# Optimization experiments

Measured on AMD Instinct MI355X. Metric: run time of the kernel, lower is better.

The kernel has to match this reference:

```python
import jax, jax.numpy as jnp
import numpy as np

SCORE_THRESHOLD = 0.5
IOU_THRESHOLD = 0.5
N = 8192
IMG = 640.0


def setup_inputs() -> dict:
    key = jax.random.key(0)
    k1, k2, k3 = jax.random.split(key, 3)
    # valid xyxy boxes on a 640px canvas: x2 > x1, y2 > y1
    xy1 = jax.random.uniform(k1, (N, 2), dtype=jnp.float32) * (IMG - 64.0)
    wh = jax.random.uniform(k2, (N, 2), dtype=jnp.float32) * 96.0 + 4.0
    xyxy = jnp.concatenate([xy1, xy1 + wh], axis=1)  # [N,4]
    person_conf = jax.random.uniform(k3, (N,), dtype=jnp.float32)  # [N]
    return {"xyxy": xyxy, "person_conf": person_conf}


def _pairwise_iou(boxes):
    # boxes: [N,4] xyxy -> iou: [N,N]
    x1, y1, x2, y2 = boxes[:, 0], boxes[:, 1], boxes[:, 2], boxes[:, 3]
    area = (x2 - x1) * (y2 - y1)  # [N]
    ix1 = jnp.maximum(x1[:, None], x1[None, :])
    iy1 = jnp.maximum(y1[:, None], y1[None, :])
    ix2 = jnp.minimum(x2[:, None], x2[None, :])
    iy2 = jnp.minimum(y2[:, None], y2[None, :])
    iw = jnp.maximum(ix2 - ix1, 0.0)
    ih = jnp.maximum(iy2 - iy1, 0.0)
    inter = iw * ih
    union = area[:, None] + area[None, :] - inter
    return inter / jnp.maximum(union, 1e-9)


def reference(xyxy, person_conf):
    # score-threshold filter (as a mask to stay jit-compatible / fixed shape)
    valid = person_conf >= SCORE_THRESHOLD  # [N]
    # sort by score descending; invalid boxes sink to the bottom
    sort_scores = jnp.where(valid, person_conf, -jnp.inf)
    order = jnp.argsort(-sort_scores)  # [N]
    boxes_s = xyxy[order]              # [N,4]
    scores_s = person_conf[order]      # [N]
    valid_s = valid[order]             # [N]

    iou = _pairwise_iou(boxes_s)  # [N,N]
    idx = jnp.arange(N)

    def body(i, keep):
        # box i (if still kept) suppresses lower-scored overlapping boxes
        sup = keep[i] & (iou[i] > IOU_THRESHOLD) & (idx > i)
        return keep & ~sup

    keep = jax.lax.fori_loop(0, N, body, valid_s)  # [N] bool

    boxes_and_scores = jnp.concatenate([boxes_s, scores_s[:, None]], axis=1)  # [N,5]
    out = jnp.where(keep[:, None], boxes_and_scores, 0.0)  # suppressed rows zeroed
    return out, keep
```

## Files before the change

kernel.cpp:

```cpp
#include <hip/hip_runtime.h>

typedef unsigned long long u64;
typedef unsigned int u32;
typedef unsigned short u16;
typedef unsigned char u8;

static constexpr int N = 8192;
static constexpr int NW = N / 64;
static constexpr int CAPE = 12288;


__device__ __forceinline__ u64 make_key(float s, int i) {
  u32 adj = (s >= 0.5f) ? (__float_as_uint(s) + 1u) : 0u;
  return ((u64)adj << 32) | (u64)(u32)(N - 1 - i);
}

__global__ __launch_bounds__(256)
void rank_kernel(const float* __restrict__ conf, u32* __restrict__ rank_partial) {
  __shared__ u64 sk[1024];
  const int t = threadIdx.x;
  const int jb = blockIdx.y;
  for (int k = t; k < 1024; k += 256) {
    int j = jb * 1024 + k;
    sk[k] = make_key(conf[j], j);
  }
  __syncthreads();
  const int i = blockIdx.x * 256 + t;
  const u64 ki = make_key(conf[i], i);
  int cnt = 0;
  #pragma unroll 8
  for (int k = 0; k < 1024; ++k) cnt += (sk[k] > ki);
  rank_partial[jb * N + i] = (u32)cnt;
}

__global__ __launch_bounds__(256)
void scatter_kernel(const float4* __restrict__ xyxy, const float* __restrict__ conf,
                    const u32* __restrict__ rank_partial,
                    float4* __restrict__ boxes_s, float* __restrict__ scores_s,
                    float* __restrict__ areas_s) {
  #pragma clang fp contract(off)
  const int i = blockIdx.x * 256 + threadIdx.x;
  u32 r = 0;
  #pragma unroll
  for (int jb = 0; jb < 8; ++jb) r += rank_partial[jb * N + i];
  float4 b = xyxy[i];
  boxes_s[r] = b;
  scores_s[r] = conf[i];
  areas_s[r] = (b.z - b.x) * (b.w - b.y);
}

__global__ __launch_bounds__(64)
void mask_kernel(const float4* __restrict__ boxes_s, const float* __restrict__ areas_s,
                 const float* __restrict__ scores_s,
                 u64* __restrict__ mask, u64* __restrict__ nzT) {
  #pragma clang fp contract(off)
  const int xb = blockIdx.x;
  const int yb = blockIdx.y;
  if (xb < yb) return;
  if (scores_s[xb * 64] < 0.5f) return;
  __shared__ float4 cb[64];
  __shared__ float ca[64];
  const int t = threadIdx.x;
  cb[t] = boxes_s[xb * 64 + t];
  ca[t] = areas_s[xb * 64 + t];
  __syncthreads();
  const int i = yb * 64 + t;
  const float4 rb = boxes_s[i];
  const float ra = areas_s[i];
  const int jbase = xb * 64;
  u64 w = 0;
  for (int q = 0; q < 64; ++q) {
    float4 c = cb[q];
    float ix1 = fmaxf(rb.x, c.x);
    float iy1 = fmaxf(rb.y, c.y);
    float ix2 = fminf(rb.z, c.z);
    float iy2 = fminf(rb.w, c.w);
    float iw = fmaxf(ix2 - ix1, 0.0f);
    float ih = fmaxf(iy2 - iy1, 0.0f);
    float inter = iw * ih;
    float uni = fmaxf((ra + ca[q]) - inter, 1e-9f);
    float iou = inter / uni;
    if ((iou > 0.5f) && (jbase + q > i)) w |= (1ull << q);
  }
  if (w) mask[(u64)i * NW + xb] = w;
  u64 nz = __ballot(w != 0ull);
  if (t == 0) nzT[(u64)xb * 128 + yb] = nz;
}

__global__ __launch_bounds__(1024)
void reduce_write_kernel(const u64* __restrict__ mask, const u64* __restrict__ nzT,
                         const float* __restrict__ scores_s,
                         const float4* __restrict__ boxes_s,
                         float* __restrict__ out) {
  __shared__ u64 words[CAPE];
  __shared__ u16 rowid[CAPE];
  __shared__ u8  xbs[CAPE];
  __shared__ u32 removed32[2 * NW];
  __shared__ u32 keep32[2 * NW];
  __shared__ u64 validm[NW];
  __shared__ int total;
  __shared__ int chg[2];
  __shared__ int VBsh;
  const int tid = threadIdx.x;
  const int lane = tid & 63;

  if (tid == 0) { total = 0; chg[0] = 0; chg[1] = 0; VBsh = 0; }
  for (int p = tid; p < N; p += 1024) {
    u64 b = __ballot(scores_s[p] >= 0.5f);
    if (lane == 0) validm[p >> 6] = b;
  }
  __syncthreads();
  if (tid < 128 && validm[tid] != 0ull) atomicMax(&VBsh, tid + 1);
  if (tid < 256) keep32[tid] = ((const u32*)validm)[tid];
  __syncthreads();
  const int VB = VBsh;

  for (int p = tid; p < 128 * 128; p += 1024) {
    int xb = p >> 7, yb = p & 127;
    if (yb > xb || xb >= VB) continue;
    u64 nz = nzT[p] & validm[yb];
    while (nz) {
      int b = __builtin_ctzll(nz); nz &= nz - 1;
      int row = yb * 64 + b;
      int idx = atomicAdd(&total, 1);
      if (idx < CAPE) {
        words[idx] = mask[(u64)row * NW + xb];
        rowid[idx] = (u16)row;
        xbs[idx] = (u8)xb;
      }
    }
  }
  __syncthreads();
  const int E = (total < CAPE) ? total : CAPE;

  for (int it = 0; it < N; ++it) {
    if (tid < 256) removed32[tid] = 0;
    if (tid == 0) chg[(it + 1) & 1] = 0;
    __syncthreads();
    for (int e = tid; e < E; e += 1024) {
      int j = rowid[e];
      if ((keep32[j >> 5] >> (j & 31)) & 1u) {
        u64 w = words[e]; int x = xbs[e];
        atomicOr(&removed32[2 * x],     (u32)w);
        atomicOr(&removed32[2 * x + 1], (u32)(w >> 32));
      }
    }
    __syncthreads();
    if (tid < 256) {
      u32 vm = ((const u32*)validm)[tid];
      u32 nk = vm & ~removed32[tid];
      if (nk != keep32[tid]) { keep32[tid] = nk; atomicOr(&chg[it & 1], 1); }
    }
    __syncthreads();
    if (!chg[it & 1]) break;
  }

  for (int s = tid; s < N; s += 1024) {
    bool keep = (keep32[s >> 5] >> (s & 31)) & 1u;
    float4 b = boxes_s[s];
    float sc = scores_s[s];
    float* row = out + (u64)s * 5;
    if (keep) {
      row[0] = b.x; row[1] = b.y; row[2] = b.z; row[3] = b.w; row[4] = sc;
      out[N * 5 + s] = 1.0f;
    } else {
      row[0] = 0.0f; row[1] = 0.0f; row[2] = 0.0f; row[3] = 0.0f; row[4] = 0.0f;
      out[N * 5 + s] = 0.0f;
    }
  }
}

extern "C" void kernel_launch(void* const* d_in, const int* in_sizes, int n_in,
                              void* d_out, int out_size, void* d_ws, size_t ws_size,
                              hipStream_t stream) {
  const float4* xyxy = (const float4*)d_in[0];
  const float* conf  = (const float*)d_in[1];
  char* ws = (char*)d_ws;
  float4* boxes_s   = (float4*)(ws + 0);
  float*  scores_s  = (float*)(ws + 131072);
  float*  areas_s   = (float*)(ws + 163840);
  u64*    nzT       = (u64*)(ws + 197632);
  u64*    mask      = (u64*)(ws + 328704);
  u32*    rank_partial = (u32*)(ws + 328704);
  float*  out       = (float*)d_out;

  dim3 rg(N / 256, 8);
  rank_kernel<<<rg, 256, 0, stream>>>(conf, rank_partial);
  scatter_kernel<<<N / 256, 256, 0, stream>>>(xyxy, conf, rank_partial,
                                              boxes_s, scores_s, areas_s);
  dim3 mg(NW, NW);
  mask_kernel<<<mg, 64, 0, stream>>>(boxes_s, areas_s, scores_s, mask, nzT);
  reduce_write_kernel<<<1, 1024, 0, stream>>>(mask, nzT, scores_s, boxes_s, out);
}
```

Baseline: 142.6 us.

## Compact suppression edges in mask kernel and keep them in registers for reduction

The mask kernel now appends only nonzero suppression words, tagged with row and column block, to a global edge list through a wave-level atomic counter. This removes the dense mask and nonzero-bitmap tables and the serial per-bit gather pass in the single-block reduce kernel. The reduce kernel loads each thread's edges into registers once and iterates the fixed-point suppression from those registers instead of shared memory. The mask kernel also packs four column blocks per 256-thread block, which lowers the block count. In exchange it adds a global atomic per wave and makes the edge order nondeterministic.

```diff
diff --git a/kernel.cpp b/kernel.cpp
--- a/kernel.cpp
+++ b/kernel.cpp
@@ -2,12 +2,11 @@
 
 typedef unsigned long long u64;
 typedef unsigned int u32;
-typedef unsigned short u16;
-typedef unsigned char u8;
 
 static constexpr int N = 8192;
 static constexpr int NW = N / 64;
 static constexpr int CAPE = 12288;
+static constexpr int EPT = CAPE / 1024;
 
 
 __device__ __forceinline__ u64 make_key(float s, int i) {
@@ -37,9 +36,10 @@
 void scatter_kernel(const float4* __restrict__ xyxy, const float* __restrict__ conf,
                     const u32* __restrict__ rank_partial,
                     float4* __restrict__ boxes_s, float* __restrict__ scores_s,
-                    float* __restrict__ areas_s) {
+                    float* __restrict__ areas_s, int* __restrict__ ecount) {
   #pragma clang fp contract(off)
   const int i = blockIdx.x * 256 + threadIdx.x;
+  if (i == 0) *ecount = 0;
   u32 r = 0;
   #pragma unroll
   for (int jb = 0; jb < 8; ++jb) r += rank_partial[jb * N + i];
@@ -49,28 +49,30 @@
   areas_s[r] = (b.z - b.x) * (b.w - b.y);
 }
 
-__global__ __launch_bounds__(64)
+__global__ __launch_bounds__(256)
 void mask_kernel(const float4* __restrict__ boxes_s, const float* __restrict__ areas_s,
                  const float* __restrict__ scores_s,
-                 u64* __restrict__ mask, u64* __restrict__ nzT) {
+                 u64* __restrict__ edgeW, u32* __restrict__ edgeM,
+                 int* __restrict__ ecount) {
   #pragma clang fp contract(off)
-  const int xb = blockIdx.x;
+  __shared__ float4 cb[4][64];
+  __shared__ float ca[4][64];
+  const int wave = threadIdx.x >> 6;
+  const int t = threadIdx.x & 63;
+  const int xb = blockIdx.x * 4 + wave;
   const int yb = blockIdx.y;
   if (xb < yb) return;
   if (scores_s[xb * 64] < 0.5f) return;
-  __shared__ float4 cb[64];
-  __shared__ float ca[64];
-  const int t = threadIdx.x;
-  cb[t] = boxes_s[xb * 64 + t];
-  ca[t] = areas_s[xb * 64 + t];
-  __syncthreads();
+  cb[wave][t] = boxes_s[xb * 64 + t];
+  ca[wave][t] = areas_s[xb * 64 + t];
   const int i = yb * 64 + t;
   const float4 rb = boxes_s[i];
   const float ra = areas_s[i];
+  const float sc_i = scores_s[i];
   const int jbase = xb * 64;
   u64 w = 0;
   for (int q = 0; q < 64; ++q) {
-    float4 c = cb[q];
+    float4 c = cb[wave][q];
     float ix1 = fmaxf(rb.x, c.x);
     float iy1 = fmaxf(rb.y, c.y);
     float ix2 = fminf(rb.z, c.z);
@@ -78,78 +80,76 @@
     float iw = fmaxf(ix2 - ix1, 0.0f);
     float ih = fmaxf(iy2 - iy1, 0.0f);
     float inter = iw * ih;
-    float uni = fmaxf((ra + ca[q]) - inter, 1e-9f);
+    float uni = fmaxf((ra + ca[wave][q]) - inter, 1e-9f);
     float iou = inter / uni;
     if ((iou > 0.5f) && (jbase + q > i)) w |= (1ull << q);
   }
-  if (w) mask[(u64)i * NW + xb] = w;
+  if (sc_i < 0.5f) w = 0;
   u64 nz = __ballot(w != 0ull);
-  if (t == 0) nzT[(u64)xb * 128 + yb] = nz;
+  if (!nz) return;
+  int base = 0;
+  if (t == 0) base = atomicAdd(ecount, __popcll(nz));
+  base = __shfl(base, 0);
+  if (w) {
+    int idx = base + __popcll(nz & ((1ull << t) - 1ull));
+    if (idx < CAPE) {
+      edgeW[idx] = w;
+      edgeM[idx] = (u32)i | ((u32)xb << 16);
+    }
+  }
 }
 
 __global__ __launch_bounds__(1024)
-void reduce_write_kernel(const u64* __restrict__ mask, const u64* __restrict__ nzT,
+void reduce_write_kernel(const u64* __restrict__ edgeW, const u32* __restrict__ edgeM,
+                         const int* __restrict__ ecount,
                          const float* __restrict__ scores_s,
                          const float4* __restrict__ boxes_s,
                          float* __restrict__ out) {
-  __shared__ u64 words[CAPE];
-  __shared__ u16 rowid[CAPE];
-  __shared__ u8  xbs[CAPE];
   __shared__ u32 removed32[2 * NW];
   __shared__ u32 keep32[2 * NW];
   __shared__ u64 validm[NW];
-  __shared__ int total;
   __shared__ int chg[2];
-  __shared__ int VBsh;
   const int tid = threadIdx.x;
   const int lane = tid & 63;
 
-  if (tid == 0) { total = 0; chg[0] = 0; chg[1] = 0; VBsh = 0; }
+  if (tid == 0) { chg[0] = 0; chg[1] = 0; }
   for (int p = tid; p < N; p += 1024) {
     u64 b = __ballot(scores_s[p] >= 0.5f);
     if (lane == 0) validm[p >> 6] = b;
   }
+  int E = *ecount;
+  if (E > CAPE) E = CAPE;
+
+  u64 ew[EPT]; u32 em[EPT]; int ne = 0;
+  #pragma unroll
+  for (int k = 0; k < EPT; ++k) {
+    int e = tid + k * 1024;
+    if (e < E) { ew[k] = edgeW[e]; em[k] = edgeM[e]; ne = k + 1; }
+    else       { ew[k] = 0; em[k] = 0; }
+  }
   __syncthreads();
-  if (tid < 128 && validm[tid] != 0ull) atomicMax(&VBsh, tid + 1);
   if (tid < 256) keep32[tid] = ((const u32*)validm)[tid];
   __syncthreads();
-  const int VB = VBsh;
-
-  for (int p = tid; p < 128 * 128; p += 1024) {
-    int xb = p >> 7, yb = p & 127;
-    if (yb > xb || xb >= VB) continue;
-    u64 nz = nzT[p] & validm[yb];
-    while (nz) {
-      int b = __builtin_ctzll(nz); nz &= nz - 1;
-      int row = yb * 64 + b;
-      int idx = atomicAdd(&total, 1);
-      if (idx < CAPE) {
-        words[idx] = mask[(u64)row * NW + xb];
-        rowid[idx] = (u16)row;
-        xbs[idx] = (u8)xb;
-      }
-    }
-  }
-  __syncthreads();
-  const int E = (total < CAPE) ? total : CAPE;
 
   for (int it = 0; it < N; ++it) {
     if (tid < 256) removed32[tid] = 0;
     if (tid == 0) chg[(it + 1) & 1] = 0;
     __syncthreads();
-    for (int e = tid; e < E; e += 1024) {
-      int j = rowid[e];
-      if ((keep32[j >> 5] >> (j & 31)) & 1u) {
-        u64 w = words[e]; int x = xbs[e];
-        atomicOr(&removed32[2 * x],     (u32)w);
-        atomicOr(&removed32[2 * x + 1], (u32)(w >> 32));
+    #pragma unroll
+    for (int k = 0; k < EPT; ++k) {
+      if (k < ne) {
+        int row = em[k] & 0xffff;
+        if ((keep32[row >> 5] >> (row & 31)) & 1u) {
+          int x = em[k] >> 16;
+          atomicOr(&removed32[2 * x],     (u32)ew[k]);
+          atomicOr(&removed32[2 * x + 1], (u32)(ew[k] >> 32));
+        }
       }
     }
     __syncthreads();
     if (tid < 256) {
-      u32 vm = ((const u32*)validm)[tid];
-      u32 nk = vm & ~removed32[tid];
-      if (nk != keep32[tid]) { keep32[tid] = nk; atomicOr(&chg[it & 1], 1); }
+      u32 nk = ((const u32*)validm)[tid] & ~removed32[tid];
+      if (nk != keep32[tid]) { keep32[tid] = nk; chg[it & 1] = 1; }
     }
     __syncthreads();
     if (!chg[it & 1]) break;
@@ -179,16 +179,19 @@
   float4* boxes_s   = (float4*)(ws + 0);
   float*  scores_s  = (float*)(ws + 131072);
   float*  areas_s   = (float*)(ws + 163840);
-  u64*    nzT       = (u64*)(ws + 197632);
-  u64*    mask      = (u64*)(ws + 328704);
-  u32*    rank_partial = (u32*)(ws + 328704);
+  int*    ecount    = (int*)(ws + 196608);
+  u64*    edgeW     = (u64*)(ws + 196672);
+  u32*    edgeM     = (u32*)(ws + 294976);
+  u32*    rank_partial = (u32*)(ws + 344128);
   float*  out       = (float*)d_out;
 
   dim3 rg(N / 256, 8);
   rank_kernel<<<rg, 256, 0, stream>>>(conf, rank_partial);
   scatter_kernel<<<N / 256, 256, 0, stream>>>(xyxy, conf, rank_partial,
-                                              boxes_s, scores_s, areas_s);
-  dim3 mg(NW, NW);
-  mask_kernel<<<mg, 64, 0, stream>>>(boxes_s, areas_s, scores_s, mask, nzT);
-  reduce_write_kernel<<<1, 1024, 0, stream>>>(mask, nzT, scores_s, boxes_s, out);
+                                              boxes_s, scores_s, areas_s, ecount);
+  dim3 mg(NW / 4, NW);
+  mask_kernel<<<mg, 256, 0, stream>>>(boxes_s, areas_s, scores_s,
+                                      edgeW, edgeM, ecount);
+  reduce_write_kernel<<<1, 1024, 0, stream>>>(edgeW, edgeM, ecount,
+                                              scores_s, boxes_s, out);
 }
```

After: 116.2 us. 18.5% less time.
